# Kernel tuning notes

Measured on AMD Instinct MI355X. Metric: run time of the kernel, lower is better.

The kernel has to match this reference:

```python
import jax, jax.numpy as jnp
import numpy as np

M, K, N, G = 64, 4096, 11008, 128  # tokens, infeatures, outfeatures, group_size
NUM_GROUPS = K // G  # 32


def _fp8_round_trip(w):
    # Simulate FP8 E4M3 storage of the quantized weight codes.
    return w.astype(jnp.float8_e4m3fn).astype(jnp.float32)


def setup_inputs() -> dict:
    key = jax.random.key(0)
    k1, k2, k3, k4 = jax.random.split(key, 4)
    x = jax.random.normal(k1, (M, K), dtype=jnp.float32)
    # FP8-representable weight codes (post round-trip, stored as f32 values)
    weight = _fp8_round_trip(jax.random.normal(k2, (N, K), dtype=jnp.float32) * 2.0)
    # Per-(out_feature, group) dequant scales, strictly positive
    weight_scale = jax.random.uniform(k3, (N, NUM_GROUPS), dtype=jnp.float32,
                                      minval=0.005, maxval=0.02)
    bias = jax.random.normal(k4, (N,), dtype=jnp.float32)
    return {"x": x, "weight": weight, "weight_scale": weight_scale, "bias": bias}


def reference(x, weight, weight_scale, bias):
    # Dequantize: each group of `G` consecutive in-features of an output row
    # shares one scale -> w_deq[o, i] = weight[o, i] * scale[o, i // G]
    n, k = weight.shape
    g = k // weight_scale.shape[1]
    w_deq = (weight.reshape(n, -1, g) * weight_scale[:, :, None]).reshape(n, k)
    # Fused dequant-matmul: out[m, o] = sum_i x[m, i] * w_deq[o, i] + bias[o]
    out = jnp.einsum("mk,nk->mn", x, w_deq) + bias
    return out
```

## Files before the change

### kernel.cpp

```cpp
#include <hip/hip_runtime.h>


#define Md 64
#define Kd 4096
#define Nd 11008
#define NGROUPS 32
#define BN 64
#define KSPLIT 8
#define KCHUNK (Kd / KSPLIT)
#define NSTAGE (KCHUNK / 64)
#define NGRP (KCHUNK / 128)
#define KBC (KCHUNK / 32)

typedef __attribute__((ext_vector_type(8))) __bf16 bf16x8;
typedef __attribute__((ext_vector_type(4))) float f32x4;

__global__ __launch_bounds__(256)
void xprep(const float* __restrict__ x, __bf16* __restrict__ xf)
{
    const int tid  = blockIdx.x * 256 + threadIdx.x;
    const int lane = tid & 63;
    const int t    = (tid >> 6) & 3;
    const int kb   = tid >> 8;
    const int row  = t * 16 + (lane & 15);
    const int col  = kb * 32 + (lane >> 4) * 8;
    const float4 a = *(const float4*)(x + (size_t)row * Kd + col);
    const float4 b = *(const float4*)(x + (size_t)row * Kd + col + 4);
    bf16x8 v = {(__bf16)a.x, (__bf16)a.y, (__bf16)a.z, (__bf16)a.w,
                (__bf16)b.x, (__bf16)b.y, (__bf16)b.z, (__bf16)b.w};
    *(bf16x8*)(xf + (size_t)tid * 8) = v;
}

__global__ __launch_bounds__(256, 4)
void qlinear_pass1(const float* __restrict__ w,
                   const __bf16* __restrict__ xf,
                   const float* __restrict__ scale,
                   float* __restrict__ ws)
{
    const int tid  = threadIdx.x;
    const int wv   = tid >> 6;
    const int lane = tid & 63;
    const int quad = lane >> 4;
    const int ln   = lane & 15;

    const int n0 = blockIdx.x * BN;
    const int ky = blockIdx.y;
    const int k0 = ky * KCHUNK;

    __shared__ alignas(16) float lds_w[2][BN * 64];

    const float* src[4];
    #pragma unroll
    for (int j = 0; j < 4; ++j) {
        const int r   = wv * 16 + j * 4 + quad;
        const int c16 = ln ^ (r & 7);
        src[j] = w + (size_t)(n0 + r) * Kd + k0 + c16 * 4;
    }

    const __bf16* xp = xf + (size_t)ky * KBC * 4 * 512 + (size_t)lane * 8;

    const int nrow = n0 + wv * 16 + ln;
    float4 sc4 = *(const float4*)(scale + (size_t)nrow * NGROUPS + ky * NGRP);
    const float sc[4] = {sc4.x, sc4.y, sc4.z, sc4.w};

    const int rr = wv * 16 + ln;
    const int rx = rr & 7;

    f32x4 acc[4];
    #pragma unroll
    for (int t = 0; t < 4; ++t) acc[t] = (f32x4){0.f, 0.f, 0.f, 0.f};

    #pragma unroll
    for (int j = 0; j < 4; ++j)
        __builtin_amdgcn_global_load_lds(
            (const __attribute__((address_space(1))) void*)src[j],
            (__attribute__((address_space(3))) void*)&lds_w[0][(wv * 4 + j) * 256],
            16, 0, 0);
    __syncthreads();

    #pragma unroll
    for (int g = 0; g < NGRP; ++g) {
        f32x4 pg[4];
        #pragma unroll
        for (int t = 0; t < 4; ++t) pg[t] = (f32x4){0.f, 0.f, 0.f, 0.f};

        #pragma unroll
        for (int half = 0; half < 2; ++half) {
            const int s   = g * 2 + half;
            const int buf = s & 1;

            if (s + 1 < NSTAGE) {
                #pragma unroll
                for (int j = 0; j < 4; ++j)
                    __builtin_amdgcn_global_load_lds(
                        (const __attribute__((address_space(1))) void*)(src[j] + (s + 1) * 64),
                        (__attribute__((address_space(3))) void*)&lds_w[buf ^ 1][(wv * 4 + j) * 256],
                        16, 0, 0);
            }

            #pragma unroll
            for (int ks = 0; ks < 2; ++ks) {
                const int kb = s * 2 + ks;
                bf16x8 xv[4];
                #pragma unroll
                for (int t = 0; t < 4; ++t)
                    xv[t] = *(const bf16x8*)(xp + ((size_t)kb * 4 + t) * 512);

                const int c0 = ks * 8 + quad * 2;
                f32x4 fa = *(const f32x4*)&lds_w[buf][rr * 64 + (((c0    ) ^ rx) << 2)];
                f32x4 fb = *(const f32x4*)&lds_w[buf][rr * 64 + (((c0 + 1) ^ rx) << 2)];
                bf16x8 wf = {(__bf16)fa.x, (__bf16)fa.y, (__bf16)fa.z, (__bf16)fa.w,
                             (__bf16)fb.x, (__bf16)fb.y, (__bf16)fb.z, (__bf16)fb.w};
                #pragma unroll
                for (int t = 0; t < 4; ++t)
                    pg[t] = __builtin_amdgcn_mfma_f32_16x16x32_bf16(xv[t], wf, pg[t],
                                                                    0, 0, 0);
            }
            __syncthreads();
        }

        const float s = sc[g];
        #pragma unroll
        for (int t = 0; t < 4; ++t)
            #pragma unroll
            for (int r = 0; r < 4; ++r)
                acc[t][r] += s * pg[t][r];
    }

    float* op = ws + ((size_t)ky * Md) * Nd + n0 + wv * 16 + ln;
    #pragma unroll
    for (int t = 0; t < 4; ++t)
        #pragma unroll
        for (int r = 0; r < 4; ++r)
            op[(size_t)(t * 16 + quad * 4 + r) * Nd] = acc[t][r];
}

__global__ __launch_bounds__(256)
void qlinear_reduce(const float* __restrict__ ws,
                    const float* __restrict__ bias,
                    float* __restrict__ out)
{
    const int i4 = blockIdx.x * 256 + threadIdx.x;
    if (i4 >= (Md * Nd) / 4) return;
    const int n = (i4 * 4) % Nd;
    float4 v = *(const float4*)(bias + n);
    #pragma unroll
    for (int ky = 0; ky < KSPLIT; ++ky) {
        float4 p = *(const float4*)(ws + (size_t)ky * Md * Nd + (size_t)i4 * 4);
        v.x += p.x; v.y += p.y; v.z += p.z; v.w += p.w;
    }
    *(float4*)(out + (size_t)i4 * 4) = v;
}

extern "C" void kernel_launch(void* const* d_in, const int* in_sizes, int n_in,
                              void* d_out, int out_size, void* d_ws, size_t ws_size,
                              hipStream_t stream) {
    const float* x     = (const float*)d_in[0];
    const float* w     = (const float*)d_in[1];
    const float* scale = (const float*)d_in[2];
    const float* bias  = (const float*)d_in[3];
    float* out = (float*)d_out;
    float* ws  = (float*)d_ws;

    __bf16* xf = (__bf16*)(ws + (size_t)KSPLIT * Md * Nd);

    xprep<<<128, 256, 0, stream>>>(x, xf);

    dim3 grid1(Nd / BN, KSPLIT);
    qlinear_pass1<<<grid1, 256, 0, stream>>>(w, xf, scale, ws);

    qlinear_reduce<<<(Md * Nd / 4 + 255) / 256, 256, 0, stream>>>(ws, bias, out);
}
```

Before: 273.8 us.

## Replace split-K workspace and reduce kernel with atomic adds into output

```diff
diff --git a/kernel.cpp b/kernel.cpp
--- a/kernel.cpp
+++ b/kernel.cpp
@@ -16,26 +16,33 @@
 typedef __attribute__((ext_vector_type(4))) float f32x4;
 
 __global__ __launch_bounds__(256)
-void xprep(const float* __restrict__ x, __bf16* __restrict__ xf)
+void prep(const float* __restrict__ x, __bf16* __restrict__ xf,
+          const float* __restrict__ bias, float* __restrict__ out)
 {
-    const int tid  = blockIdx.x * 256 + threadIdx.x;
-    const int lane = tid & 63;
-    const int t    = (tid >> 6) & 3;
-    const int kb   = tid >> 8;
-    const int row  = t * 16 + (lane & 15);
-    const int col  = kb * 32 + (lane >> 4) * 8;
-    const float4 a = *(const float4*)(x + (size_t)row * Kd + col);
-    const float4 b = *(const float4*)(x + (size_t)row * Kd + col + 4);
-    bf16x8 v = {(__bf16)a.x, (__bf16)a.y, (__bf16)a.z, (__bf16)a.w,
-                (__bf16)b.x, (__bf16)b.y, (__bf16)b.z, (__bf16)b.w};
-    *(bf16x8*)(xf + (size_t)tid * 8) = v;
+    if (blockIdx.x < 128) {
+        const int tid  = blockIdx.x * 256 + threadIdx.x;
+        const int lane = tid & 63;
+        const int t    = (tid >> 6) & 3;
+        const int kb   = tid >> 8;
+        const int row  = t * 16 + (lane & 15);
+        const int col  = kb * 32 + (lane >> 4) * 8;
+        const float4 a = *(const float4*)(x + (size_t)row * Kd + col);
+        const float4 b = *(const float4*)(x + (size_t)row * Kd + col + 4);
+        bf16x8 v = {(__bf16)a.x, (__bf16)a.y, (__bf16)a.z, (__bf16)a.w,
+                    (__bf16)b.x, (__bf16)b.y, (__bf16)b.z, (__bf16)b.w};
+        *(bf16x8*)(xf + (size_t)tid * 8) = v;
+    } else {
+        const int i4 = (blockIdx.x - 128) * 256 + threadIdx.x;
+        const int n  = (i4 * 4) % Nd;
+        *(float4*)(out + (size_t)i4 * 4) = *(const float4*)(bias + n);
+    }
 }
 
 __global__ __launch_bounds__(256, 4)
 void qlinear_pass1(const float* __restrict__ w,
                    const __bf16* __restrict__ xf,
                    const float* __restrict__ scale,
-                   float* __restrict__ ws)
+                   float* __restrict__ out)
 {
     const int tid  = threadIdx.x;
     const int wv   = tid >> 6;
@@ -127,29 +134,12 @@
                 acc[t][r] += s * pg[t][r];
     }
 
-    float* op = ws + ((size_t)ky * Md) * Nd + n0 + wv * 16 + ln;
+    float* op = out + n0 + wv * 16 + ln;
     #pragma unroll
     for (int t = 0; t < 4; ++t)
         #pragma unroll
         for (int r = 0; r < 4; ++r)
-            op[(size_t)(t * 16 + quad * 4 + r) * Nd] = acc[t][r];
-}
-
-__global__ __launch_bounds__(256)
-void qlinear_reduce(const float* __restrict__ ws,
-                    const float* __restrict__ bias,
-                    float* __restrict__ out)
-{
-    const int i4 = blockIdx.x * 256 + threadIdx.x;
-    if (i4 >= (Md * Nd) / 4) return;
-    const int n = (i4 * 4) % Nd;
-    float4 v = *(const float4*)(bias + n);
-    #pragma unroll
-    for (int ky = 0; ky < KSPLIT; ++ky) {
-        float4 p = *(const float4*)(ws + (size_t)ky * Md * Nd + (size_t)i4 * 4);
-        v.x += p.x; v.y += p.y; v.z += p.z; v.w += p.w;
-    }
-    *(float4*)(out + (size_t)i4 * 4) = v;
+            unsafeAtomicAdd(&op[(size_t)(t * 16 + quad * 4 + r) * Nd], acc[t][r]);
 }
 
 extern "C" void kernel_launch(void* const* d_in, const int* in_sizes, int n_in,
@@ -162,12 +152,10 @@
     float* out = (float*)d_out;
     float* ws  = (float*)d_ws;
 
-    __bf16* xf = (__bf16*)(ws + (size_t)KSPLIT * Md * Nd);
+    __bf16* xf = (__bf16*)ws;
 
-    xprep<<<128, 256, 0, stream>>>(x, xf);
+    prep<<<816, 256, 0, stream>>>(x, xf, bias, out);
 
     dim3 grid1(Nd / BN, KSPLIT);
-    qlinear_pass1<<<grid1, 256, 0, stream>>>(w, xf, scale, ws);
-
-    qlinear_reduce<<<(Md * Nd / 4 + 255) / 256, 256, 0, stream>>>(ws, bias, out);
+    qlinear_pass1<<<grid1, 256, 0, stream>>>(w, xf, scale, out);
 }
```

After: 269.2 us. Within noise of the previous version (-1.7%).
